# Kernel optimization log

Measured on AMD Instinct MI355X. Metric: run time of the kernel, lower is better.

Reference implementation:

```python
import jax, jax.numpy as jnp
import numpy as np

HIDDEN = 1024
N_HEAD = 16
HEAD_DIM = HIDDEN // N_HEAD


def setup_inputs() -> dict:
    key = jax.random.key(0)
    ks = jax.random.split(key, 11)
    B, S, D, H, E = 4, 1024, HIDDEN, N_HEAD, HEAD_DIM
    sc = 0.02
    return {
        "query": jax.random.normal(ks[0], (B, S, D), jnp.float32),
        "key": jax.random.normal(ks[1], (B, S, D), jnp.float32),
        "value": jax.random.normal(ks[2], (B, S, D), jnp.float32),
        # per-head projection weights stacked over heads (torch Linear: y = x @ W.T + b)
        "Wq": jax.random.normal(ks[3], (H, D, E), jnp.float32) * sc,
        "bq": jax.random.normal(ks[4], (H, E), jnp.float32) * sc,
        "Wk": jax.random.normal(ks[5], (H, D, E), jnp.float32) * sc,
        "bk": jax.random.normal(ks[6], (H, E), jnp.float32) * sc,
        "Wv": jax.random.normal(ks[7], (H, D, E), jnp.float32) * sc,
        "bv": jax.random.normal(ks[8], (H, E), jnp.float32) * sc,
        "Wo": jax.random.normal(ks[9], (D, D), jnp.float32) * sc,
        "bo": jax.random.normal(ks[10], (D,), jnp.float32) * sc,
    }


def reference(query, key, value, Wq, bq, Wk, bk, Wv, bv, Wo, bo):
    B, S, D = query.shape
    H, _, E = Wq.shape
    # per-head linear projections (vectorized over heads)
    q = jnp.einsum("bsd,hde->bhse", query, Wq) + bq[None, :, None, :]
    k = jnp.einsum("bsd,hde->bhse", key, Wk) + bk[None, :, None, :]
    v = jnp.einsum("bsd,hde->bhse", value, Wv) + bv[None, :, None, :]
    scale = jnp.sqrt(jnp.asarray(E, q.dtype))
    scores = jnp.einsum("bhse,bhte->bhst", q, k) / scale  # [B,H,S,S]
    attn = jax.nn.softmax(scores, axis=-1)  # dropout is identity in eval
    wv = jnp.einsum("bhst,bhte->bhse", attn, v)  # [B,H,S,E]
    # concat heads along feature dim (head h -> slice h*E:(h+1)*E)
    wv = wv.transpose(0, 2, 1, 3).reshape(B, S, H * E)
    out = wv @ Wo.T + bo  # final linear; output dropout identity in eval
    return out
```

## Files before the change

kernel.cpp:

```cpp
#include <hip/hip_runtime.h>

typedef unsigned short u16;
typedef unsigned int u32;
typedef __attribute__((ext_vector_type(8))) short bf16x8;
typedef __attribute__((ext_vector_type(4))) float f32x4;

#define B_SZ 4
#define S_SZ 1024
#define D_SZ 1024
#define H_SZ 16
#define E_SZ 64
#define M_SZ (B_SZ * S_SZ)

__device__ __forceinline__ u16 f2bf(float f) {
  union { float f; unsigned u; } x; x.f = f;
  unsigned r = (x.u + 0x7FFFu + ((x.u >> 16) & 1u)) >> 16;
  return (u16)r;
}

__device__ __forceinline__ u32 pack_bf16(float lo, float hi) {
  return (u32)f2bf(lo) | ((u32)f2bf(hi) << 16);
}

__device__ __forceinline__ void async16(const void* g, void* l) {
  __builtin_amdgcn_global_load_lds(
      (const __attribute__((address_space(1))) void*)g,
      (__attribute__((address_space(3))) void*)l, 16, 0, 0);
}

__device__ __forceinline__ f32x4 mfma16(bf16x8 a, bf16x8 b, f32x4 c) {
  return __builtin_amdgcn_mfma_f32_16x16x32_bf16(a, b, c, 0, 0, 0);
}

__global__ void cast4(const float* __restrict__ q, const float* __restrict__ k,
                      const float* __restrict__ v, const float* __restrict__ Wo,
                      u16* __restrict__ oq, u16* __restrict__ ok,
                      u16* __restrict__ ov, u16* __restrict__ oWo) {
  int gid = blockIdx.x * 256 + threadIdx.x;
  const float* in;
  u16* out;
  int i;
  if (gid < (3 << 19)) {
    int sel = gid >> 19;
    i = (gid & ((1 << 19) - 1)) << 3;
    in = sel == 0 ? q : (sel == 1 ? k : v);
    out = sel == 0 ? oq : (sel == 1 ? ok : ov);
  } else {
    i = (gid - (3 << 19)) << 3;
    in = Wo;
    out = oWo;
  }
  float4 a = *(const float4*)(in + i);
  float4 b = *(const float4*)(in + i + 4);
  alignas(16) u16 r[8];
  r[0] = f2bf(a.x); r[1] = f2bf(a.y); r[2] = f2bf(a.z); r[3] = f2bf(a.w);
  r[4] = f2bf(b.x); r[5] = f2bf(b.y); r[6] = f2bf(b.z); r[7] = f2bf(b.w);
  *(uint4*)(out + i) = *(uint4*)r;
}

__global__ void transW3(const float* __restrict__ Wq, const float* __restrict__ Wk,
                        const float* __restrict__ Wv, u16* __restrict__ Tq,
                        u16* __restrict__ Tk, u16* __restrict__ Tv) {
  __shared__ float tile[64 * 68];
  const int wsel = blockIdx.x >> 8;
  const int bi = blockIdx.x & 255;
  const float* W = wsel == 0 ? Wq : (wsel == 1 ? Wk : Wv);
  u16* WT = wsel == 0 ? Tq : (wsel == 1 ? Tk : Tv);
  const int tid = threadIdx.x;
  const int h = bi >> 4;
  const int d0 = (bi & 15) << 6;
#pragma unroll
  for (int c = 0; c < 4; ++c) {
    const int dd = c * 16 + (tid >> 4);
    const int e4 = (tid & 15) << 2;
    float4 vq = *(const float4*)(W + (h << 16) + ((d0 + dd) << 6) + e4);
    *(float4*)(tile + dd * 68 + e4) = vq;
  }
  __syncthreads();
  {
    const int e = tid >> 2;
    const int dc = (tid & 3) << 4;
    alignas(16) u16 outv[16];
#pragma unroll
    for (int i = 0; i < 16; ++i) outv[i] = f2bf(tile[(dc + i) * 68 + e]);
    u16* dst = WT + (((size_t)(h << 6) + e) << 10) + d0 + dc;
    *(uint4*)(dst) = *(uint4*)outv;
    *(uint4*)(dst + 8) = *(uint4*)(outv + 8);
  }
}

__global__ __launch_bounds__(256)
void gemm3(const u16* __restrict__ qb, const u16* __restrict__ kb, const u16* __restrict__ vb,
           const u16* __restrict__ Tq, const u16* __restrict__ Tk, const u16* __restrict__ Tv,
           const float* __restrict__ bq, const float* __restrict__ bk, const float* __restrict__ bv,
           u16* __restrict__ Qp, u16* __restrict__ Kp, u16* __restrict__ VpT) {
  __shared__ u16 Al[2][128 * 64];
  __shared__ u16 Bl[2][128 * 64];
  const int wg = blockIdx.x;
  const int swz = (wg & 7) * 96 + (wg >> 3);
  const int g = swz >> 8;
  const int bi = swz & 255;
  const u16* A = g == 0 ? qb : (g == 1 ? kb : vb);
  const u16* BT = g == 0 ? Tq : (g == 1 ? Tk : Tv);
  const float* bias = g == 0 ? bq : (g == 1 ? bk : bv);
  u16* Cout = g == 0 ? Qp : (g == 1 ? Kp : VpT);
  const float scale = g == 0 ? 0.125f : 1.0f;

  const int tid = threadIdx.x;
  const int wave = tid >> 6;
  const int lane = tid & 63;
  const int l15 = lane & 15, lq = lane >> 4;
  const int bm = bi >> 3;
  const int bn = bi & 7;
  const int row0 = bm << 7, col0 = bn << 7;
  const int wr = ((wave >> 1) & 1) << 6;
  const int wc = (wave & 1) << 6;

  int xs[4], rowS[4], cbS[4];
#pragma unroll
  for (int c = 0; c < 4; ++c) {
    int x = c * 4096 + tid * 16;
    int gx = x ^ (((x >> 7) & 7) << 4);
    xs[c] = x;
    rowS[c] = gx >> 7;
    cbS[c] = (gx & 127) >> 1;
  }

  f32x4 acc[4][4];
#pragma unroll
  for (int m = 0; m < 4; ++m)
#pragma unroll
    for (int n = 0; n < 4; ++n) acc[m][n] = (f32x4)0.0f;

#pragma unroll
  for (int c = 0; c < 4; ++c) {
    async16(A + (size_t)(row0 + rowS[c]) * 1024 + cbS[c], (char*)Al[0] + xs[c]);
    async16(BT + (size_t)(col0 + rowS[c]) * 1024 + cbS[c], (char*)Bl[0] + xs[c]);
  }
  __syncthreads();

  int buf = 0;
  for (int k0 = 0; k0 < 1024; k0 += 64) {
    if (k0 + 64 < 1024) {
      const int kn = k0 + 64;
#pragma unroll
      for (int c = 0; c < 4; ++c) {
        async16(A + (size_t)(row0 + rowS[c]) * 1024 + kn + cbS[c], (char*)Al[buf ^ 1] + xs[c]);
        async16(BT + (size_t)(col0 + rowS[c]) * 1024 + kn + cbS[c], (char*)Bl[buf ^ 1] + xs[c]);
      }
    }

    bf16x8 af[4][2], bfr[4][2];
#pragma unroll
    for (int m = 0; m < 4; ++m)
#pragma unroll
      for (int kf = 0; kf < 2; ++kf) {
        int r = wr + m * 16 + l15;
        int byte = ((r << 7) + kf * 64 + lq * 16) ^ ((r & 7) << 4);
        af[m][kf] = *(const bf16x8*)((const char*)Al[buf] + byte);
      }
#pragma unroll
    for (int n = 0; n < 4; ++n)
#pragma unroll
      for (int kf = 0; kf < 2; ++kf) {
        int r = wc + n * 16 + l15;
        int byte = ((r << 7) + kf * 64 + lq * 16) ^ ((r & 7) << 4);
        bfr[n][kf] = *(const bf16x8*)((const char*)Bl[buf] + byte);
      }
    if (g == 2) {
#pragma unroll
      for (int kf = 0; kf < 2; ++kf)
#pragma unroll
        for (int m = 0; m < 4; ++m)
#pragma unroll
          for (int n = 0; n < 4; ++n)
            acc[m][n] = mfma16(af[m][kf], bfr[n][kf], acc[m][n]);
    } else {
#pragma unroll
      for (int kf = 0; kf < 2; ++kf)
#pragma unroll
        for (int m = 0; m < 4; ++m)
#pragma unroll
          for (int n = 0; n < 4; ++n)
            acc[m][n] = mfma16(bfr[n][kf], af[m][kf], acc[m][n]);
    }

    __syncthreads();
    buf ^= 1;
  }

  if (g == 2) {
#pragma unroll
    for (int m = 0; m < 4; ++m)
#pragma unroll
      for (int n = 0; n < 4; ++n) {
        int col = col0 + wc + n * 16 + l15;
        float bv = bias[col];
        int rowb = row0 + wr + m * 16 + lq * 4;
        alignas(8) u16 r4[4];
#pragma unroll
        for (int j = 0; j < 4; ++j) r4[j] = f2bf(acc[m][n][j] + bv);
        *(uint2*)(Cout + (size_t)col * 4096 + rowb) = *(uint2*)r4;
      }
  } else {
    float4 b4[4];
#pragma unroll
    for (int n = 0; n < 4; ++n)
      b4[n] = *(const float4*)(bias + col0 + wc + n * 16 + lq * 4);
#pragma unroll
    for (int m = 0; m < 4; ++m) {
      int row = row0 + wr + m * 16 + l15;
#pragma unroll
      for (int n = 0; n < 4; ++n) {
        int colbase = col0 + wc + n * 16 + lq * 4;
        u32 lo = pack_bf16((acc[m][n][0] + b4[n].x) * scale,
                           (acc[m][n][1] + b4[n].y) * scale);
        u32 hi = pack_bf16((acc[m][n][2] + b4[n].z) * scale,
                           (acc[m][n][3] + b4[n].w) * scale);
        uint2 wv; wv.x = lo; wv.y = hi;
        *(uint2*)(Cout + (size_t)row * 1024 + colbase) = wv;
      }
    }
  }
}

__global__ __launch_bounds__(512, 4)
void gemmO8(const u16* __restrict__ A, const u16* __restrict__ BT,
            const float* __restrict__ bias, float* __restrict__ out) {
  __shared__ u16 Al[2][128 * 64];
  __shared__ u16 Bl[2][128 * 64];
  const int tid = threadIdx.x;
  const int wave = tid >> 6;
  const int lane = tid & 63;
  const int l15 = lane & 15, lq = lane >> 4;
  const int wg = blockIdx.x;
  const int bi = (wg & 7) * 32 + (wg >> 3);
  const int bm = bi >> 3;
  const int bn = bi & 7;
  const int row0 = bm << 7, col0 = bn << 7;
  const int wr = (wave >> 1) << 5;
  const int wc = (wave & 1) << 6;

  int xs[2], rowS[2], cbS[2];
#pragma unroll
  for (int c = 0; c < 2; ++c) {
    int x = c * 8192 + tid * 16;
    int gx = x ^ (((x >> 7) & 7) << 4);
    xs[c] = x;
    rowS[c] = gx >> 7;
    cbS[c] = (gx & 127) >> 1;
  }

  f32x4 acc[2][4];
#pragma unroll
  for (int m = 0; m < 2; ++m)
#pragma unroll
    for (int n = 0; n < 4; ++n) acc[m][n] = (f32x4)0.0f;

#pragma unroll
  for (int c = 0; c < 2; ++c) {
    async16(A + (size_t)(row0 + rowS[c]) * 1024 + cbS[c], (char*)Al[0] + xs[c]);
    async16(BT + (size_t)(col0 + rowS[c]) * 1024 + cbS[c], (char*)Bl[0] + xs[c]);
  }
  __syncthreads();

  int buf = 0;
  for (int k0 = 0; k0 < 1024; k0 += 64) {
    if (k0 + 64 < 1024) {
      const int kn = k0 + 64;
#pragma unroll
      for (int c = 0; c < 2; ++c) {
        async16(A + (size_t)(row0 + rowS[c]) * 1024 + kn + cbS[c], (char*)Al[buf ^ 1] + xs[c]);
        async16(BT + (size_t)(col0 + rowS[c]) * 1024 + kn + cbS[c], (char*)Bl[buf ^ 1] + xs[c]);
      }
    }

    bf16x8 af[2][2], bfr[4][2];
#pragma unroll
    for (int m = 0; m < 2; ++m)
#pragma unroll
      for (int kf = 0; kf < 2; ++kf) {
        int r = wr + m * 16 + l15;
        int byte = ((r << 7) + kf * 64 + lq * 16) ^ ((r & 7) << 4);
        af[m][kf] = *(const bf16x8*)((const char*)Al[buf] + byte);
      }
#pragma unroll
    for (int n = 0; n < 4; ++n)
#pragma unroll
      for (int kf = 0; kf < 2; ++kf) {
        int r = wc + n * 16 + l15;
        int byte = ((r << 7) + kf * 64 + lq * 16) ^ ((r & 7) << 4);
        bfr[n][kf] = *(const bf16x8*)((const char*)Bl[buf] + byte);
      }
#pragma unroll
    for (int kf = 0; kf < 2; ++kf)
#pragma unroll
      for (int m = 0; m < 2; ++m)
#pragma unroll
        for (int n = 0; n < 4; ++n)
          acc[m][n] = mfma16(bfr[n][kf], af[m][kf], acc[m][n]);

    __syncthreads();
    buf ^= 1;
  }

  float4 b4[4];
#pragma unroll
  for (int n = 0; n < 4; ++n)
    b4[n] = *(const float4*)(bias + col0 + wc + n * 16 + lq * 4);
#pragma unroll
  for (int m = 0; m < 2; ++m) {
    int row = row0 + wr + m * 16 + l15;
#pragma unroll
    for (int n = 0; n < 4; ++n) {
      int colbase = col0 + wc + n * 16 + lq * 4;
      float4 v;
      v.x = acc[m][n][0] + b4[n].x;
      v.y = acc[m][n][1] + b4[n].y;
      v.z = acc[m][n][2] + b4[n].z;
      v.w = acc[m][n][3] + b4[n].w;
      *(float4*)(out + (size_t)row * 1024 + colbase) = v;
    }
  }
}

__global__ __launch_bounds__(256)
void attn(const u16* __restrict__ Qp, const u16* __restrict__ Kp,
          const u16* __restrict__ VpT, u16* __restrict__ Ow) {
  __shared__ alignas(16) u16 Kl[2][64 * 64];
  __shared__ alignas(16) u16 VTl[2][64 * 64];
  __shared__ alignas(16) u16 Pl[4][16 * 64];
  const int tid = threadIdx.x;
  const int wave = tid >> 6;
  const int lane = tid & 63;
  const int l15 = lane & 15, lq = lane >> 4;
  const int wg = blockIdx.x;
  const int swz = (wg & 7) * 128 + (wg >> 3);
  const int qt = swz & 15;
  const int bh = swz >> 4;
  const int b = bh >> 4, h = bh & 15;
  const size_t bS = (size_t)b * S_SZ;

  const int xs0 = tid * 16, xs1 = 4096 + tid * 16;
  const int r0 = xs0 >> 7, r1 = xs1 >> 7;
  const int c0 = ((xs0 & 127) ^ (((xs0 >> 7) & 7) << 4)) >> 1;
  const int c1 = ((xs1 & 127) ^ (((xs1 >> 7) & 7) << 4)) >> 1;
  const u16* Kb0 = Kp + ((bS + r0) << 10) + h * 64 + c0;
  const u16* Kb1 = Kp + ((bS + r1) << 10) + h * 64 + c1;
  const u16* Vb0 = VpT + (size_t)(h * 64 + r0) * 4096 + bS + c0;
  const u16* Vb1 = VpT + (size_t)(h * 64 + r1) * 4096 + bS + c1;

  bf16x8 aq[2];
  {
    const u16* qptr = Qp + ((bS + qt * 64 + wave * 16 + l15) << 10) + h * 64 + lq * 8;
    aq[0] = *(const bf16x8*)(qptr);
    aq[1] = *(const bf16x8*)(qptr + 32);
  }

  f32x4 o[4];
#pragma unroll
  for (int n = 0; n < 4; ++n) o[n] = (f32x4)0.0f;
  float m_run = -1e30f;
  float l_run = 0.f;
  u16* Pw = Pl[wave];

  async16(Kb0, (char*)Kl[0] + xs0);
  async16(Kb1, (char*)Kl[0] + xs1);
  async16(Vb0, (char*)VTl[0] + xs0);
  async16(Vb1, (char*)VTl[0] + xs1);
  __syncthreads();

  int buf = 0;
  for (int t0 = 0; t0 < S_SZ; t0 += 64) {
    if (t0 + 64 < S_SZ) {
      const int tn = t0 + 64;
      async16(Kb0 + ((size_t)tn << 10), (char*)Kl[buf ^ 1] + xs0);
      async16(Kb1 + ((size_t)tn << 10), (char*)Kl[buf ^ 1] + xs1);
      async16(Vb0 + tn, (char*)VTl[buf ^ 1] + xs0);
      async16(Vb1 + tn, (char*)VTl[buf ^ 1] + xs1);
    }

    f32x4 s[4];
#pragma unroll
    for (int n = 0; n < 4; ++n) s[n] = (f32x4)0.0f;
    __builtin_amdgcn_s_setprio(1);
#pragma unroll
    for (int n = 0; n < 4; ++n)
#pragma unroll
      for (int kf = 0; kf < 2; ++kf) {
        int r = n * 16 + l15;
        int byte = ((r << 7) + kf * 64 + lq * 16) ^ ((r & 7) << 4);
        bf16x8 bk = *(const bf16x8*)((const char*)Kl[buf] + byte);
        s[n] = mfma16(bk, aq[kf], s[n]);
      }
    __builtin_amdgcn_s_setprio(0);

    float mx = s[0][0];
#pragma unroll
    for (int n = 0; n < 4; ++n)
#pragma unroll
      for (int j = 0; j < 4; ++j) mx = fmaxf(mx, s[n][j]);
    mx = fmaxf(mx, __shfl_xor(mx, 16, 64));
    mx = fmaxf(mx, __shfl_xor(mx, 32, 64));

    if (__any(mx > m_run + 8.0f)) {
      float mn = fmaxf(m_run, mx);
      float alpha = __expf(m_run - mn);
      m_run = mn;
      l_run *= alpha;
      float a0 = __shfl(alpha, lq * 4 + 0, 64);
      float a1 = __shfl(alpha, lq * 4 + 1, 64);
      float a2 = __shfl(alpha, lq * 4 + 2, 64);
      float a3 = __shfl(alpha, lq * 4 + 3, 64);
#pragma unroll
      for (int n = 0; n < 4; ++n) {
        o[n][0] *= a0; o[n][1] *= a1; o[n][2] *= a2; o[n][3] *= a3;
      }
    }

    float rs = 0.f;
#pragma unroll
    for (int n = 0; n < 4; ++n) {
      float p0 = __expf(s[n][0] - m_run);
      float p1 = __expf(s[n][1] - m_run);
      float p2 = __expf(s[n][2] - m_run);
      float p3 = __expf(s[n][3] - m_run);
      rs += (p0 + p1) + (p2 + p3);
      u32 lo = pack_bf16(p0, p1);
      u32 hi = pack_bf16(p2, p3);
      int byte = (l15 << 7) + (((n * 32 + lq * 8)) ^ ((l15 & 7) << 4));
      uint2 wv; wv.x = lo; wv.y = hi;
      *(uint2*)((char*)Pw + byte) = wv;
    }
    rs += __shfl_xor(rs, 16, 64);
    rs += __shfl_xor(rs, 32, 64);
    l_run += rs;

    __builtin_amdgcn_s_setprio(1);
#pragma unroll
    for (int kf = 0; kf < 2; ++kf) {
      int pbyte = (l15 << 7) + ((kf * 64 + lq * 16) ^ ((l15 & 7) << 4));
      bf16x8 pa = *(const bf16x8*)((const char*)Pw + pbyte);
#pragma unroll
      for (int n = 0; n < 4; ++n) {
        int vr = n * 16 + l15;
        int byte = ((vr << 7) + kf * 64 + lq * 16) ^ ((vr & 7) << 4);
        bf16x8 bv = *(const bf16x8*)((const char*)VTl[buf] + byte);
        o[n] = mfma16(pa, bv, o[n]);
      }
    }
    __builtin_amdgcn_s_setprio(0);

    __syncthreads();
    buf ^= 1;
  }

  float li0 = __shfl(l_run, lq * 4 + 0, 64);
  float li1 = __shfl(l_run, lq * 4 + 1, 64);
  float li2 = __shfl(l_run, lq * 4 + 2, 64);
  float li3 = __shfl(l_run, lq * 4 + 3, 64);
  float inv0 = 1.0f / li0, inv1 = 1.0f / li1, inv2 = 1.0f / li2, inv3 = 1.0f / li3;
#pragma unroll
  for (int n = 0; n < 4; ++n) {
    float vals[4] = {o[n][0] * inv0, o[n][1] * inv1, o[n][2] * inv2, o[n][3] * inv3};
#pragma unroll
    for (int j = 0; j < 4; ++j) {
      int row = qt * 64 + wave * 16 + lq * 4 + j;
      int col = h * 64 + n * 16 + l15;
      Ow[((bS + row) << 10) + col] = f2bf(vals[j]);
    }
  }
}

extern "C" void kernel_launch(void* const* d_in, const int* in_sizes, int n_in,
                              void* d_out, int out_size, void* d_ws, size_t ws_size,
                              hipStream_t stream) {
  const float* q  = (const float*)d_in[0];
  const float* k  = (const float*)d_in[1];
  const float* v  = (const float*)d_in[2];
  const float* Wq = (const float*)d_in[3];
  const float* bq = (const float*)d_in[4];
  const float* Wk = (const float*)d_in[5];
  const float* bk = (const float*)d_in[6];
  const float* Wv = (const float*)d_in[7];
  const float* bv = (const float*)d_in[8];
  const float* Wo = (const float*)d_in[9];
  const float* bo = (const float*)d_in[10];

  char* w = (char*)d_ws;
  const size_t MB = 1u << 20;
  u16* qb  = (u16*)(w + 0 * MB);
  u16* kb  = (u16*)(w + 8 * MB);
  u16* vb  = (u16*)(w + 16 * MB);
  u16* WqT = (u16*)(w + 24 * MB);
  u16* WkT = (u16*)(w + 26 * MB);
  u16* WvT = (u16*)(w + 28 * MB);
  u16* Wob = (u16*)(w + 30 * MB);
  u16* Qp  = (u16*)(w + 32 * MB);
  u16* Kp  = (u16*)(w + 40 * MB);
  u16* VpT = (u16*)(w + 48 * MB);
  u16* wvb = (u16*)(w + 56 * MB);

  cast4<<<6656, 256, 0, stream>>>(q, k, v, Wo, qb, kb, vb, Wob);
  transW3<<<768, 256, 0, stream>>>(Wq, Wk, Wv, WqT, WkT, WvT);

  gemm3<<<768, 256, 0, stream>>>(qb, kb, vb, WqT, WkT, WvT, bq, bk, bv, Qp, Kp, VpT);

  attn<<<B_SZ * H_SZ * (S_SZ / 64), 256, 0, stream>>>(Qp, Kp, VpT, wvb);

  gemmO8<<<256, 512, 0, stream>>>(wvb, Wob, bo, (float*)d_out);
}
```

Measured before the change: 122.2 us.

## Process two query subtiles per wave in attention; single-buffer gemm3 loads

```diff
diff --git a/kernel.cpp b/kernel.cpp
--- a/kernel.cpp
+++ b/kernel.cpp
@@ -94,8 +94,8 @@
            const u16* __restrict__ Tq, const u16* __restrict__ Tk, const u16* __restrict__ Tv,
            const float* __restrict__ bq, const float* __restrict__ bk, const float* __restrict__ bv,
            u16* __restrict__ Qp, u16* __restrict__ Kp, u16* __restrict__ VpT) {
-  __shared__ u16 Al[2][128 * 64];
-  __shared__ u16 Bl[2][128 * 64];
+  __shared__ u16 Al[128 * 64];
+  __shared__ u16 Bl[128 * 64];
   const int wg = blockIdx.x;
   const int swz = (wg & 7) * 96 + (wg >> 3);
   const int g = swz >> 8;
@@ -116,39 +116,26 @@
   const int wr = ((wave >> 1) & 1) << 6;
   const int wc = (wave & 1) << 6;
 
-  int xs[4], rowS[4], cbS[4];
-#pragma unroll
-  for (int c = 0; c < 4; ++c) {
-    int x = c * 4096 + tid * 16;
-    int gx = x ^ (((x >> 7) & 7) << 4);
-    xs[c] = x;
-    rowS[c] = gx >> 7;
-    cbS[c] = (gx & 127) >> 1;
-  }
-
   f32x4 acc[4][4];
 #pragma unroll
   for (int m = 0; m < 4; ++m)
 #pragma unroll
     for (int n = 0; n < 4; ++n) acc[m][n] = (f32x4)0.0f;
 
-#pragma unroll
-  for (int c = 0; c < 4; ++c) {
-    async16(A + (size_t)(row0 + rowS[c]) * 1024 + cbS[c], (char*)Al[0] + xs[c]);
-    async16(BT + (size_t)(col0 + rowS[c]) * 1024 + cbS[c], (char*)Bl[0] + xs[c]);
-  }
-  __syncthreads();
-
-  int buf = 0;
   for (int k0 = 0; k0 < 1024; k0 += 64) {
-    if (k0 + 64 < 1024) {
-      const int kn = k0 + 64;
-#pragma unroll
-      for (int c = 0; c < 4; ++c) {
-        async16(A + (size_t)(row0 + rowS[c]) * 1024 + kn + cbS[c], (char*)Al[buf ^ 1] + xs[c]);
-        async16(BT + (size_t)(col0 + rowS[c]) * 1024 + kn + cbS[c], (char*)Bl[buf ^ 1] + xs[c]);
-      }
-    }
+    __syncthreads();
+#pragma unroll
+    for (int c = 0; c < 4; ++c) {
+      const int x = c * 4096 + tid * 16;
+      const int gx = x ^ (((x >> 7) & 7) << 4);
+      const int row = gx >> 7;
+      const int cb = gx & 127;
+      const u16* ga = A + (size_t)(row0 + row) * 1024 + k0 + (cb >> 1);
+      const u16* gb = BT + (size_t)(col0 + row) * 1024 + k0 + (cb >> 1);
+      async16(ga, (char*)Al + x);
+      async16(gb, (char*)Bl + x);
+    }
+    __syncthreads();
 
     bf16x8 af[4][2], bfr[4][2];
 #pragma unroll
@@ -157,7 +144,7 @@
       for (int kf = 0; kf < 2; ++kf) {
         int r = wr + m * 16 + l15;
         int byte = ((r << 7) + kf * 64 + lq * 16) ^ ((r & 7) << 4);
-        af[m][kf] = *(const bf16x8*)((const char*)Al[buf] + byte);
+        af[m][kf] = *(const bf16x8*)((const char*)Al + byte);
       }
 #pragma unroll
     for (int n = 0; n < 4; ++n)
@@ -165,7 +152,7 @@
       for (int kf = 0; kf < 2; ++kf) {
         int r = wc + n * 16 + l15;
         int byte = ((r << 7) + kf * 64 + lq * 16) ^ ((r & 7) << 4);
-        bfr[n][kf] = *(const bf16x8*)((const char*)Bl[buf] + byte);
+        bfr[n][kf] = *(const bf16x8*)((const char*)Bl + byte);
       }
     if (g == 2) {
 #pragma unroll
@@ -184,9 +171,6 @@
           for (int n = 0; n < 4; ++n)
             acc[m][n] = mfma16(bfr[n][kf], af[m][kf], acc[m][n]);
     }
-
-    __syncthreads();
-    buf ^= 1;
   }
 
   if (g == 2) {
@@ -329,15 +313,15 @@
           const u16* __restrict__ VpT, u16* __restrict__ Ow) {
   __shared__ alignas(16) u16 Kl[2][64 * 64];
   __shared__ alignas(16) u16 VTl[2][64 * 64];
-  __shared__ alignas(16) u16 Pl[4][16 * 64];
+  __shared__ alignas(16) u16 Pl[4][2][16 * 64];
   const int tid = threadIdx.x;
   const int wave = tid >> 6;
   const int lane = tid & 63;
   const int l15 = lane & 15, lq = lane >> 4;
   const int wg = blockIdx.x;
-  const int swz = (wg & 7) * 128 + (wg >> 3);
-  const int qt = swz & 15;
-  const int bh = swz >> 4;
+  const int swz = (wg & 7) * 64 + (wg >> 3);
+  const int qt = swz & 7;
+  const int bh = swz >> 3;
   const int b = bh >> 4, h = bh & 15;
   const size_t bS = (size_t)b * S_SZ;
 
@@ -350,19 +334,23 @@
   const u16* Vb0 = VpT + (size_t)(h * 64 + r0) * 4096 + bS + c0;
   const u16* Vb1 = VpT + (size_t)(h * 64 + r1) * 4096 + bS + c1;
 
-  bf16x8 aq[2];
+  bf16x8 aq0[2], aq1[2];
   {
-    const u16* qptr = Qp + ((bS + qt * 64 + wave * 16 + l15) << 10) + h * 64 + lq * 8;
-    aq[0] = *(const bf16x8*)(qptr);
-    aq[1] = *(const bf16x8*)(qptr + 32);
-  }
-
-  f32x4 o[4];
-#pragma unroll
-  for (int n = 0; n < 4; ++n) o[n] = (f32x4)0.0f;
-  float m_run = -1e30f;
-  float l_run = 0.f;
-  u16* Pw = Pl[wave];
+    const u16* qp0 = Qp + ((bS + qt * 128 + wave * 32 + l15) << 10) + h * 64 + lq * 8;
+    aq0[0] = *(const bf16x8*)(qp0);
+    aq0[1] = *(const bf16x8*)(qp0 + 32);
+    const u16* qp1 = qp0 + (16 << 10);
+    aq1[0] = *(const bf16x8*)(qp1);
+    aq1[1] = *(const bf16x8*)(qp1 + 32);
+  }
+
+  f32x4 o0[4], o1[4];
+#pragma unroll
+  for (int n = 0; n < 4; ++n) { o0[n] = (f32x4)0.0f; o1[n] = (f32x4)0.0f; }
+  float m0 = -1e30f, m1 = -1e30f;
+  float l0 = 0.f, l1 = 0.f;
+  u16* Pw0 = Pl[wave][0];
+  u16* Pw1 = Pl[wave][1];
 
   async16(Kb0, (char*)Kl[0] + xs0);
   async16(Kb1, (char*)Kl[0] + xs1);
@@ -380,9 +368,9 @@
       async16(Vb1 + tn, (char*)VTl[buf ^ 1] + xs1);
     }
 
-    f32x4 s[4];
-#pragma unroll
-    for (int n = 0; n < 4; ++n) s[n] = (f32x4)0.0f;
+    f32x4 s0[4], s1[4];
+#pragma unroll
+    for (int n = 0; n < 4; ++n) { s0[n] = (f32x4)0.0f; s1[n] = (f32x4)0.0f; }
     __builtin_amdgcn_s_setprio(1);
 #pragma unroll
     for (int n = 0; n < 4; ++n)
@@ -391,62 +379,105 @@
         int r = n * 16 + l15;
         int byte = ((r << 7) + kf * 64 + lq * 16) ^ ((r & 7) << 4);
         bf16x8 bk = *(const bf16x8*)((const char*)Kl[buf] + byte);
-        s[n] = mfma16(bk, aq[kf], s[n]);
+        s0[n] = mfma16(bk, aq0[kf], s0[n]);
+        s1[n] = mfma16(bk, aq1[kf], s1[n]);
       }
     __builtin_amdgcn_s_setprio(0);
 
-    float mx = s[0][0];
-#pragma unroll
-    for (int n = 0; n < 4; ++n)
-#pragma unroll
-      for (int j = 0; j < 4; ++j) mx = fmaxf(mx, s[n][j]);
-    mx = fmaxf(mx, __shfl_xor(mx, 16, 64));
-    mx = fmaxf(mx, __shfl_xor(mx, 32, 64));
-
-    if (__any(mx > m_run + 8.0f)) {
-      float mn = fmaxf(m_run, mx);
-      float alpha = __expf(m_run - mn);
-      m_run = mn;
-      l_run *= alpha;
-      float a0 = __shfl(alpha, lq * 4 + 0, 64);
-      float a1 = __shfl(alpha, lq * 4 + 1, 64);
-      float a2 = __shfl(alpha, lq * 4 + 2, 64);
-      float a3 = __shfl(alpha, lq * 4 + 3, 64);
+    {
+      float mx = s0[0][0];
+#pragma unroll
+      for (int n = 0; n < 4; ++n)
+#pragma unroll
+        for (int j = 0; j < 4; ++j) mx = fmaxf(mx, s0[n][j]);
+      mx = fmaxf(mx, __shfl_xor(mx, 16, 64));
+      mx = fmaxf(mx, __shfl_xor(mx, 32, 64));
+      if (__any(mx > m0 + 8.0f)) {
+        float mn = fmaxf(m0, mx);
+        float alpha = __expf(m0 - mn);
+        m0 = mn;
+        l0 *= alpha;
+        float a0 = __shfl(alpha, lq * 4 + 0, 64);
+        float a1 = __shfl(alpha, lq * 4 + 1, 64);
+        float a2 = __shfl(alpha, lq * 4 + 2, 64);
+        float a3 = __shfl(alpha, lq * 4 + 3, 64);
+#pragma unroll
+        for (int n = 0; n < 4; ++n) {
+          o0[n][0] *= a0; o0[n][1] *= a1; o0[n][2] *= a2; o0[n][3] *= a3;
+        }
+      }
+      float rs = 0.f;
 #pragma unroll
       for (int n = 0; n < 4; ++n) {
-        o[n][0] *= a0; o[n][1] *= a1; o[n][2] *= a2; o[n][3] *= a3;
-      }
-    }
-
-    float rs = 0.f;
-#pragma unroll
-    for (int n = 0; n < 4; ++n) {
-      float p0 = __expf(s[n][0] - m_run);
-      float p1 = __expf(s[n][1] - m_run);
-      float p2 = __expf(s[n][2] - m_run);
-      float p3 = __expf(s[n][3] - m_run);
-      rs += (p0 + p1) + (p2 + p3);
-      u32 lo = pack_bf16(p0, p1);
-      u32 hi = pack_bf16(p2, p3);
-      int byte = (l15 << 7) + (((n * 32 + lq * 8)) ^ ((l15 & 7) << 4));
-      uint2 wv; wv.x = lo; wv.y = hi;
-      *(uint2*)((char*)Pw + byte) = wv;
-    }
-    rs += __shfl_xor(rs, 16, 64);
-    rs += __shfl_xor(rs, 32, 64);
-    l_run += rs;
+        float p0 = __expf(s0[n][0] - m0);
+        float p1 = __expf(s0[n][1] - m0);
+        float p2 = __expf(s0[n][2] - m0);
+        float p3 = __expf(s0[n][3] - m0);
+        rs += (p0 + p1) + (p2 + p3);
+        u32 lo = pack_bf16(p0, p1);
+        u32 hi = pack_bf16(p2, p3);
+        int byte = (l15 << 7) + (((n * 32 + lq * 8)) ^ ((l15 & 7) << 4));
+        uint2 wv; wv.x = lo; wv.y = hi;
+        *(uint2*)((char*)Pw0 + byte) = wv;
+      }
+      rs += __shfl_xor(rs, 16, 64);
+      rs += __shfl_xor(rs, 32, 64);
+      l0 += rs;
+    }
+    {
+      float mx = s1[0][0];
+#pragma unroll
+      for (int n = 0; n < 4; ++n)
+#pragma unroll
+        for (int j = 0; j < 4; ++j) mx = fmaxf(mx, s1[n][j]);
+      mx = fmaxf(mx, __shfl_xor(mx, 16, 64));
+      mx = fmaxf(mx, __shfl_xor(mx, 32, 64));
+      if (__any(mx > m1 + 8.0f)) {
+        float mn = fmaxf(m1, mx);
+        float alpha = __expf(m1 - mn);
+        m1 = mn;
+        l1 *= alpha;
+        float a0 = __shfl(alpha, lq * 4 + 0, 64);
+        float a1 = __shfl(alpha, lq * 4 + 1, 64);
+        float a2 = __shfl(alpha, lq * 4 + 2, 64);
+        float a3 = __shfl(alpha, lq * 4 + 3, 64);
+#pragma unroll
+        for (int n = 0; n < 4; ++n) {
+          o1[n][0] *= a0; o1[n][1] *= a1; o1[n][2] *= a2; o1[n][3] *= a3;
+        }
+      }
+      float rs = 0.f;
+#pragma unroll
+      for (int n = 0; n < 4; ++n) {
+        float p0 = __expf(s1[n][0] - m1);
+        float p1 = __expf(s1[n][1] - m1);
+        float p2 = __expf(s1[n][2] - m1);
+        float p3 = __expf(s1[n][3] - m1);
+        rs += (p0 + p1) + (p2 + p3);
+        u32 lo = pack_bf16(p0, p1);
+        u32 hi = pack_bf16(p2, p3);
+        int byte = (l15 << 7) + (((n * 32 + lq * 8)) ^ ((l15 & 7) << 4));
+        uint2 wv; wv.x = lo; wv.y = hi;
+        *(uint2*)((char*)Pw1 + byte) = wv;
+      }
+      rs += __shfl_xor(rs, 16, 64);
+      rs += __shfl_xor(rs, 32, 64);
+      l1 += rs;
+    }
 
     __builtin_amdgcn_s_setprio(1);
 #pragma unroll
     for (int kf = 0; kf < 2; ++kf) {
       int pbyte = (l15 << 7) + ((kf * 64 + lq * 16) ^ ((l15 & 7) << 4));
-      bf16x8 pa = *(const bf16x8*)((const char*)Pw + pbyte);
+      bf16x8 pa0 = *(const bf16x8*)((const char*)Pw0 + pbyte);
+      bf16x8 pa1 = *(const bf16x8*)((const char*)Pw1 + pbyte);
 #pragma unroll
       for (int n = 0; n < 4; ++n) {
         int vr = n * 16 + l15;
         int byte = ((vr << 7) + kf * 64 + lq * 16) ^ ((vr & 7) << 4);
         bf16x8 bv = *(const bf16x8*)((const char*)VTl[buf] + byte);
-        o[n] = mfma16(pa, bv, o[n]);
+        o0[n] = mfma16(pa0, bv, o0[n]);
+        o1[n] = mfma16(pa1, bv, o1[n]);
       }
     }
     __builtin_amdgcn_s_setprio(0);
@@ -455,19 +486,24 @@
     buf ^= 1;
   }
 
-  float li0 = __shfl(l_run, lq * 4 + 0, 64);
-  float li1 = __shfl(l_run, lq * 4 + 1, 64);
-  float li2 = __shfl(l_run, lq * 4 + 2, 64);
-  float li3 = __shfl(l_run, lq * 4 + 3, 64);
-  float inv0 = 1.0f / li0, inv1 = 1.0f / li1, inv2 = 1.0f / li2, inv3 = 1.0f / li3;
-#pragma unroll
-  for (int n = 0; n < 4; ++n) {
-    float vals[4] = {o[n][0] * inv0, o[n][1] * inv1, o[n][2] * inv2, o[n][3] * inv3};
-#pragma unroll
-    for (int j = 0; j < 4; ++j) {
-      int row = qt * 64 + wave * 16 + lq * 4 + j;
-      int col = h * 64 + n * 16 + l15;
-      Ow[((bS + row) << 10) + col] = f2bf(vals[j]);
+#pragma unroll
+  for (int qg = 0; qg < 2; ++qg) {
+    float lr = qg == 0 ? l0 : l1;
+    f32x4* o = qg == 0 ? o0 : o1;
+    float li0 = __shfl(lr, lq * 4 + 0, 64);
+    float li1 = __shfl(lr, lq * 4 + 1, 64);
+    float li2 = __shfl(lr, lq * 4 + 2, 64);
+    float li3 = __shfl(lr, lq * 4 + 3, 64);
+    float inv0 = 1.0f / li0, inv1 = 1.0f / li1, inv2 = 1.0f / li2, inv3 = 1.0f / li3;
+#pragma unroll
+    for (int n = 0; n < 4; ++n) {
+      float vals[4] = {o[n][0] * inv0, o[n][1] * inv1, o[n][2] * inv2, o[n][3] * inv3};
+#pragma unroll
+      for (int j = 0; j < 4; ++j) {
+        int row = qt * 128 + wave * 32 + qg * 16 + lq * 4 + j;
+        int col = h * 64 + n * 16 + l15;
+        Ow[((bS + row) << 10) + col] = f2bf(vals[j]);
+      }
     }
   }
 }
@@ -506,7 +542,7 @@
 
   gemm3<<<768, 256, 0, stream>>>(qb, kb, vb, WqT, WkT, WvT, bq, bk, bv, Qp, Kp, VpT);
 
-  attn<<<B_SZ * H_SZ * (S_SZ / 64), 256, 0, stream>>>(Qp, Kp, VpT, wvb);
+  attn<<<512, 256, 0, stream>>>(Qp, Kp, VpT, wvb);
 
   gemmO8<<<256, 512, 0, stream>>>(wvb, Wob, bo, (float*)d_out);
 }
```

Measured after the change: 121.7 us. About the same (-0.4%).
